# Kernel tuning notes

Measured on AMD Instinct MI355X. Metric: run time of the kernel, lower is better.

## Reference

```python
import jax, jax.numpy as jnp
import numpy as np

N_NODES = 50000
N_EDGES = 1600000
N_GRAPHS = 512
IN_DIM = 128
HID = 128          # nb_hidden
HALF = HID // 2    # per-branch GAT out dim
NEG_SLOPE = 0.2


def _glorot(key, shape):
    fan_in, fan_out = shape[0], shape[-1]
    lim = (6.0 / (fan_in + fan_out)) ** 0.5
    return jax.random.uniform(key, shape, jnp.float32, -lim, lim)


def setup_inputs() -> dict:
    key = jax.random.key(0)
    ks = jax.random.split(key, 32)
    inp = {
        "x": jax.random.normal(ks[0], (N_NODES, IN_DIM), jnp.float32),
        "edge_index": jax.random.randint(ks[1], (2, N_EDGES), 0, N_NODES, jnp.int64),
        "dense_edge_idx": jax.random.randint(ks[2], (2, N_EDGES), 0, N_NODES, jnp.int64),
        "batch": jnp.sort(jax.random.randint(ks[3], (N_NODES,), 0, N_GRAPHS, jnp.int64)),
    }
    # Shared GAT layers (layersB aliases layersA in the source!), nb_layer = 3
    in_dims = [IN_DIM, HID, HID]
    for i, d_in in enumerate(in_dims):
        inp[f"W{i}"] = _glorot(ks[4 + 4 * i], (d_in, HALF))
        inp[f"a_src{i}"] = _glorot(ks[5 + 4 * i], (1, HALF))[0]
        inp[f"a_dst{i}"] = _glorot(ks[6 + 4 * i], (1, HALF))[0]
        inp[f"b{i}"] = jnp.zeros((HALF,), jnp.float32)
    inp["Wf"] = _glorot(ks[20], (HID, 1))
    inp["bf"] = jnp.zeros((1,), jnp.float32)
    return inp


def _gat_conv(x, src, dst, W, a_src, a_dst, b):
    """PyG GATConv, heads=1, concat=True, add_self_loops=True."""
    n = x.shape[0]
    h = x @ W                                   # [N, HALF]
    loops = jnp.arange(n, dtype=src.dtype)
    s = jnp.concatenate([src, loops])           # [E+N]
    d = jnp.concatenate([dst, loops])
    e = (h @ a_src)[s] + (h @ a_dst)[d]         # per-edge raw score
    e = jnp.where(e >= 0, e, NEG_SLOPE * e)     # LeakyReLU(0.2)
    # segment softmax over destination nodes
    m = jax.ops.segment_max(e, d, num_segments=n)
    e = jnp.exp(e - m[d])
    z = jax.ops.segment_sum(e, d, num_segments=n)
    alpha = e / (z[d] + 1e-16)                  # [E+N]
    out = jax.ops.segment_sum(h[s] * alpha[:, None], d, num_segments=n)
    return out + b


def reference(x, edge_index, dense_edge_idx, batch,
              W0, a_src0, a_dst0, b0,
              W1, a_src1, a_dst1, b1,
              W2, a_src2, a_dst2, b2,
              Wf, bf):
    layers = [(W0, a_src0, a_dst0, b0), (W1, a_src1, a_dst1, b1), (W2, a_src2, a_dst2, b2)]
    for (W, a_s, a_d, b) in layers:
        x_A = _gat_conv(x, edge_index[0], edge_index[1], W, a_s, a_d, b)
        x_B = _gat_conv(x, dense_edge_idx[0], dense_edge_idx[1], W, a_s, a_d, b)
        x = jax.nn.relu(jnp.concatenate([x_A, x_B], axis=1))   # [N, HID]
    pooled = jax.ops.segment_sum(x, batch, num_segments=N_GRAPHS)  # [G, HID]
    y = (pooled @ Wf + bf).squeeze(-1)                             # [G]
    return y
```

## Files before the change

kernel.cpp:

```cpp
#include <hip/hip_runtime.h>
#include <hip/hip_bf16.h>
#include <hip/hip_fp16.h>

#define NEG_INF -3.4e38f
#define BCAP 9216

typedef _Float16 f16x8 __attribute__((ext_vector_type(8)));
typedef float f32x4 __attribute__((ext_vector_type(4)));

static __device__ __forceinline__ float leaky(float t) { return t >= 0.f ? t : 0.2f * t; }
static __device__ __forceinline__ float4 h4tof4(uint2 u) {
    float2 f01 = __half22float2(*(__half2*)&u.x);
    float2 f23 = __half22float2(*(__half2*)&u.y);
    return make_float4(f01.x, f01.y, f23.x, f23.y);
}

__global__ __launch_bounds__(256) void bucket_k(const int* __restrict__ eiA, const int* __restrict__ eiB,
                                                int E, int nbkt, int* __restrict__ bktCnt,
                                                int* __restrict__ pairs,
                                                const float* __restrict__ W0, const float* __restrict__ W1,
                                                const float* __restrict__ W2, _Float16* __restrict__ Wt) {
    int t = threadIdx.x;
    if (blockIdx.x < 96) {
        int i = blockIdx.x * 256 + t;
        int l = i >> 13;
        int idx = i & 8191;
        int c = idx >> 7;
        int k = idx & 127;
        const float* W = (l == 0) ? W0 : (l == 1) ? W1 : W2;
        Wt[i] = (_Float16)W[k * 64 + c];
    }

    int KB = gridDim.x >> 1;
    int b = blockIdx.x;
    int sel = (b >= KB);
    int bb = sel ? b - KB : b;
    const int* src = sel ? eiB : eiA;
    const int* dst = src + E;
    int* bc = bktCnt + (sel ? nbkt : 0);
    int* pr = pairs + (size_t)(sel ? nbkt : 0) * BCAP;

    __shared__ int hist[256];
    hist[t] = 0;
    __syncthreads();

    int e0 = (int)(((long long)bb * E) / KB);
    int e1 = (int)(((long long)(bb + 1) * E) / KB);
    for (int i = e0 + t; i < e1; i += 256) atomicAdd(&hist[dst[i] >> 8], 1);
    __syncthreads();

    int h = hist[t];
    int base = h ? atomicAdd(&bc[t], h) : 0;
    __syncthreads();
    hist[t] = base;
    __syncthreads();

    for (int i = e0 + t; i < e1; i += 256) {
        int d = dst[i];
        int s = src[i];
        int bk = d >> 8;
        int pos = atomicAdd(&hist[bk], 1);
        if (pos < BCAP) pr[(size_t)bk * BCAP + pos] = s | ((d & 255) << 16);
    }
}

__global__ __launch_bounds__(256) void bscan_k(const int* __restrict__ bktCnt, const int* __restrict__ pairs,
                                               int N, int nbkt, int2* __restrict__ rpl2,
                                               int* __restrict__ bsum) {
    __shared__ int h[256];
    int b = blockIdx.x;
    int sel = (b >= nbkt);
    int bk = sel ? b - nbkt : b;
    const int* bc = bktCnt + (sel ? nbkt : 0);
    const int* pr = pairs + ((size_t)(sel ? nbkt : 0) + bk) * BCAP;
    int t = threadIdx.x;
    h[t] = 0;
    __syncthreads();
    int cb = min(bc[bk], BCAP);
    for (int i = t; i < cb; i += 256) atomicAdd(&h[pr[i] >> 16], 1);
    __syncthreads();
    int v = h[t];
#pragma unroll
    for (int off = 1; off < 256; off <<= 1) {
        int add = (t >= off) ? h[t - off] : 0;
        __syncthreads();
        h[t] += add;
        __syncthreads();
    }
    int node = (bk << 8) + t;
    if (node < N) rpl2[(sel ? N : 0) + node] = make_int2(h[t] - v, v);
    if (t == 255) bsum[b] = h[255];
}

__global__ __launch_bounds__(512) void scan2_k(int* __restrict__ bsum, int nb,
                                               float* __restrict__ y, const float* __restrict__ bf, int G) {
    __shared__ int s[512];
    int t = threadIdx.x;
    for (int g = t; g < G; g += 512) y[g] = bf[0];
    int seg = t >> 8;
    int j = t & 255;
    int v = (j < nb) ? bsum[seg * nb + j] : 0;
    s[t] = v;
    __syncthreads();
#pragma unroll
    for (int off = 1; off < 256; off <<= 1) {
        int add = (j >= off) ? s[t - off] : 0;
        __syncthreads();
        s[t] += add;
        __syncthreads();
    }
    if (j < nb) bsum[seg * nb + j] = s[t] - v;
}

__global__ __launch_bounds__(256) void bfill2_k(const int* __restrict__ bktCnt, const int* __restrict__ pairs,
                                                int N, int nbkt, const int2* __restrict__ rpl2,
                                                const int* __restrict__ bsum, int4* __restrict__ meta,
                                                int* __restrict__ colA, int* __restrict__ colB) {
    __shared__ int curs[256];
    int b = blockIdx.x;
    int sel = (b >= nbkt);
    int bk = sel ? b - nbkt : b;
    const int* bc = bktCnt + (sel ? nbkt : 0);
    const int* pr = pairs + ((size_t)(sel ? nbkt : 0) + bk) * BCAP;
    int* col = sel ? colB : colA;
    int t = threadIdx.x;
    int base = bsum[b];
    int node = (bk << 8) + t;
    if (node < N) {
        int2 lv = rpl2[(sel ? N : 0) + node];
        int r0 = lv.x + base;
        *(int2*)&meta[(sel ? N : 0) + node] = make_int2(r0, lv.y);
        curs[t] = r0;
    }
    __syncthreads();
    int cb = min(bc[bk], BCAP);
    for (int i = t; i < cb; i += 256) {
        int pk = pr[i];
        int p = atomicAdd(&curs[pk >> 16], 1);
        col[p] = pk & 0xFFFF;
    }
}

template <int IN16>
__global__ __launch_bounds__(256) void gemm_k(const void* __restrict__ Xv, const _Float16* __restrict__ Wt,
                                              const float* __restrict__ asrc, const float* __restrict__ adst,
                                              _Float16* __restrict__ H16, int4* __restrict__ metaA,
                                              int4* __restrict__ metaB, int N) {
    int tid = threadIdx.x;
    int w = tid >> 6;
    int lane = tid & 63;
    int l15 = lane & 15;
    int hi = lane >> 4;
    int rbase = blockIdx.x * 128 + w * 32;

    f32x4 acc[2][4] = {};
#pragma unroll
    for (int kc = 0; kc < 4; ++kc) {
        f16x8 a[2];
#pragma unroll
        for (int mt = 0; mt < 2; ++mt) {
            int r = min(rbase + mt * 16 + l15, N - 1);
            if (IN16) {
                const _Float16* X = (const _Float16*)Xv;
                a[mt] = *(const f16x8*)(X + (size_t)r * 128 + kc * 32 + hi * 8);
            } else {
                const float* px = (const float*)Xv + (size_t)r * 128 + kc * 32 + hi * 8;
                float4 x0 = *(const float4*)px;
                float4 x1 = *(const float4*)(px + 4);
                f16x8 t;
                t[0] = (_Float16)x0.x; t[1] = (_Float16)x0.y; t[2] = (_Float16)x0.z; t[3] = (_Float16)x0.w;
                t[4] = (_Float16)x1.x; t[5] = (_Float16)x1.y; t[6] = (_Float16)x1.z; t[7] = (_Float16)x1.w;
                a[mt] = t;
            }
        }
#pragma unroll
        for (int nt = 0; nt < 4; ++nt) {
            f16x8 bfrag = *(const f16x8*)(Wt + (size_t)(nt * 16 + l15) * 128 + kc * 32 + hi * 8);
            acc[0][nt] = __builtin_amdgcn_mfma_f32_16x16x32_f16(a[0], bfrag, acc[0][nt], 0, 0, 0);
            acc[1][nt] = __builtin_amdgcn_mfma_f32_16x16x32_f16(a[1], bfrag, acc[1][nt], 0, 0, 0);
        }
    }

    float av[4], dv[4];
#pragma unroll
    for (int nt = 0; nt < 4; ++nt) {
        av[nt] = asrc[nt * 16 + l15];
        dv[nt] = adst[nt * 16 + l15];
    }
#pragma unroll
    for (int mt = 0; mt < 2; ++mt) {
#pragma unroll
        for (int r = 0; r < 4; ++r) {
            int row = rbase + mt * 16 + hi * 4 + r;
            float s1 = 0.f, s2 = 0.f;
#pragma unroll
            for (int nt = 0; nt < 4; ++nt) {
                float v = acc[mt][nt][r];
                s1 += v * av[nt];
                s2 += v * dv[nt];
            }
#pragma unroll
            for (int off = 1; off < 16; off <<= 1) {
                s1 += __shfl_xor(s1, off, 64);
                s2 += __shfl_xor(s2, off, 64);
            }
            if (row < N) {
                if (l15 == 0) {
                    float2 sd = make_float2(s1, s2);
                    *(float2*)((char*)&metaA[row] + 8) = sd;
                    *(float2*)((char*)&metaB[row] + 8) = sd;
                }
#pragma unroll
                for (int nt = 0; nt < 4; ++nt)
                    H16[(size_t)row * 64 + nt * 16 + l15] = (_Float16)acc[mt][nt][r];
            }
        }
    }
}

template <int WRITEY>
__global__ __launch_bounds__(256) void agg_k(const _Float16* __restrict__ h16,
                                             const float* __restrict__ asrc,
                                             const int4* __restrict__ metaA, const int* __restrict__ colA,
                                             const int4* __restrict__ metaB, const int* __restrict__ colB,
                                             const float* __restrict__ bias, __half* __restrict__ xout, int N,
                                             const float* __restrict__ Wf,
                                             float* __restrict__ ydotA, float* __restrict__ ydotB) {
    int WBh = gridDim.x >> 1;
    int b = blockIdx.x;
    int sel = (b >= WBh);
    int w = threadIdx.x >> 6;
    int lane = threadIdx.x & 63;
    int wid = (sel ? b - WBh : b) * 4 + w;
    if (wid >= N) return;
    const int4* meta = sel ? metaB : metaA;
    const int* col = sel ? colB : colA;
    int coff = sel ? 64 : 0;

    int q = lane >> 4;
    int l16 = lane & 15;
    int4 mv = meta[wid];
    int r0 = mv.x;
    int deg = mv.y;
    float esv = __int_as_float(mv.z);
    float edv = __int_as_float(mv.w);
    float m = leaky(esv + edv);
    float4 a4 = *(const float4*)(asrc + l16 * 4);

    uint2 hs = *(const uint2*)(h16 + (size_t)wid * 64 + l16 * 4);
    float4 fs = h4tof4(hs);
    float ps = (q == 0) ? 1.f : 0.f;
    float4 acc = make_float4(ps * fs.x, ps * fs.y, ps * fs.z, ps * fs.w);
    float z = ps;

    if (deg > 0) {
        int dm1 = deg - 1;
        int c1 = col[r0 + min(q, dm1)];
        int c2 = col[r0 + min(4 + q, dm1)];
        uint2 h1 = *(const uint2*)(h16 + (size_t)c1 * 64 + l16 * 4);
        uint2 h2 = *(const uint2*)(h16 + (size_t)c2 * 64 + l16 * 4);
        int n1 = col[r0 + min(8 + q, dm1)];
        int n2 = col[r0 + min(12 + q, dm1)];
        for (int j = 0; j < deg; j += 8) {
            uint2 hn1 = *(const uint2*)(h16 + (size_t)n1 * 64 + l16 * 4);
            uint2 hn2 = *(const uint2*)(h16 + (size_t)n2 * 64 + l16 * 4);
            int m1 = col[r0 + min(j + 16 + q, dm1)];
            int m2 = col[r0 + min(j + 20 + q, dm1)];

            float4 f1 = h4tof4(h1);
            float4 f2 = h4tof4(h2);
            float d1 = f1.x * a4.x + f1.y * a4.y + f1.z * a4.z + f1.w * a4.w;
            float d2 = f2.x * a4.x + f2.y * a4.y + f2.z * a4.z + f2.w * a4.w;
#pragma unroll
            for (int off = 1; off < 16; off <<= 1) {
                d1 += __shfl_xor(d1, off, 64);
                d2 += __shfl_xor(d2, off, 64);
            }
            float p1 = (j + q < deg) ? __expf(leaky(d1 + edv) - m) : 0.f;
            float p2 = (j + 4 + q < deg) ? __expf(leaky(d2 + edv) - m) : 0.f;
            z += p1 + p2;
            acc.x = fmaf(p1, f1.x, acc.x);
            acc.y = fmaf(p1, f1.y, acc.y);
            acc.z = fmaf(p1, f1.z, acc.z);
            acc.w = fmaf(p1, f1.w, acc.w);
            acc.x = fmaf(p2, f2.x, acc.x);
            acc.y = fmaf(p2, f2.y, acc.y);
            acc.z = fmaf(p2, f2.z, acc.z);
            acc.w = fmaf(p2, f2.w, acc.w);

            h1 = hn1; h2 = hn2;
            n1 = m1; n2 = m2;
        }
    }

    z += __shfl_xor(z, 16, 64);
    z += __shfl_xor(z, 32, 64);
    acc.x += __shfl_xor(acc.x, 16, 64);
    acc.y += __shfl_xor(acc.y, 16, 64);
    acc.z += __shfl_xor(acc.z, 16, 64);
    acc.w += __shfl_xor(acc.w, 16, 64);
    acc.x += __shfl_xor(acc.x, 32, 64);
    acc.y += __shfl_xor(acc.y, 32, 64);
    acc.z += __shfl_xor(acc.z, 32, 64);
    acc.w += __shfl_xor(acc.w, 32, 64);

    if (q == 0) {
        float inv = 1.f / (z + 1e-16f);
        float4 b4 = *(const float4*)(bias + l16 * 4);
        float4 o;
        o.x = fmaxf(acc.x * inv + b4.x, 0.f);
        o.y = fmaxf(acc.y * inv + b4.y, 0.f);
        o.z = fmaxf(acc.z * inv + b4.z, 0.f);
        o.w = fmaxf(acc.w * inv + b4.w, 0.f);
        if (!WRITEY) {
            __half2 o01 = __floats2half2_rn(o.x, o.y);
            __half2 o23 = __floats2half2_rn(o.z, o.w);
            uint2 st;
            st.x = *(unsigned*)&o01;
            st.y = *(unsigned*)&o23;
            *(uint2*)(xout + (size_t)wid * 128 + coff + l16 * 4) = st;
        } else {
            float4 w4 = *(const float4*)(Wf + coff + l16 * 4);
            float hd = o.x * w4.x + o.y * w4.y + o.z * w4.z + o.w * w4.w;
            hd += __shfl_xor(hd, 1, 64);
            hd += __shfl_xor(hd, 2, 64);
            hd += __shfl_xor(hd, 4, 64);
            hd += __shfl_xor(hd, 8, 64);
            if (l16 == 0) (sel ? ydotB : ydotA)[wid] = hd;
        }
    }
}

__global__ __launch_bounds__(256) void pool3_k(const float* __restrict__ ydotA, const float* __restrict__ ydotB,
                                               const int* __restrict__ batch, float* __restrict__ y,
                                               int N, int G) {
    __shared__ float gacc[512];
    int t = threadIdx.x;
    if (G <= 512) {
        for (int g = t; g < 512; g += 256) gacc[g] = 0.f;
        __syncthreads();
        int n0 = blockIdx.x * 2048 + t * 8;
        int curg = -1;
        float accv = 0.f;
        for (int i = 0; i < 8; ++i) {
            int n = n0 + i;
            if (n < N) {
                float v = ydotA[n] + ydotB[n];
                int g = batch[n];
                if (g == curg) accv += v;
                else {
                    if (curg >= 0) atomicAdd(&gacc[curg], accv);
                    curg = g;
                    accv = v;
                }
            }
        }
        if (curg >= 0) atomicAdd(&gacc[curg], accv);
        __syncthreads();
        for (int g = t; g < G; g += 256) {
            float v = gacc[g];
            if (v != 0.f) atomicAdd(&y[g], v);
        }
    } else {
        int n0 = blockIdx.x * 2048 + t * 8;
        for (int i = 0; i < 8; ++i) {
            int n = n0 + i;
            if (n < N) atomicAdd(&y[batch[n]], ydotA[n] + ydotB[n]);
        }
    }
}

static inline size_t align256(size_t x) { return (x + 255) & ~(size_t)255; }

extern "C" void kernel_launch(void* const* d_in, const int* in_sizes, int n_in,
                              void* d_out, int out_size, void* d_ws, size_t ws_size,
                              hipStream_t stream) {
    const float* x0    = (const float*)d_in[0];
    const int*   eiA   = (const int*)d_in[1];
    const int*   eiB   = (const int*)d_in[2];
    const int*   batch = (const int*)d_in[3];
    const float* W[3]   = {(const float*)d_in[4],  (const float*)d_in[8],  (const float*)d_in[12]};
    const float* as_[3] = {(const float*)d_in[5],  (const float*)d_in[9],  (const float*)d_in[13]};
    const float* ad_[3] = {(const float*)d_in[6],  (const float*)d_in[10], (const float*)d_in[14]};
    const float* bb[3]  = {(const float*)d_in[7],  (const float*)d_in[11], (const float*)d_in[15]};
    const float* Wf = (const float*)d_in[16];
    const float* bf = (const float*)d_in[17];

    const int N = in_sizes[0] / 128;
    const int E = in_sizes[1] / 2;
    const int G = out_size;
    float* y = (float*)d_out;

    const int nbkt = (N + 255) >> 8;
    const int nb = nbkt;

    char* p = (char*)d_ws;
    int2* rpl2  = (int2*)p; p += align256((size_t)2 * N * 8);
    int4* meta  = (int4*)p; p += align256((size_t)2 * N * 16);
    int* bsum   = (int*)p;  p += align256((size_t)2 * nb * 4);
    int* bktCnt = (int*)p;  p += align256((size_t)2 * nbkt * 4);
    int* colA   = (int*)p;  p += align256((size_t)E * 4);
    int* colB   = (int*)p;  p += align256((size_t)E * 4);
    _Float16* h16 = (_Float16*)p; p += align256((size_t)N * 64 * 2);
    float* ydotA = (float*)p; p += align256((size_t)N * 4);
    float* ydotB = (float*)p; p += align256((size_t)N * 4);
    _Float16* Wt = (_Float16*)p; p += align256((size_t)3 * 8192 * 2);
    __half* xb0 = (__half*)p; p += align256((size_t)N * 128 * 2);
    __half* xb1 = (__half*)p; p += align256((size_t)N * 128 * 2);
    int* pairs = (int*)xb0;
    (void)ws_size; (void)n_in;

    const int KB = 256;
    const int WB = (N + 3) / 4;
    const int PB3 = (N + 2047) / 2048;

    hipMemsetAsync(bktCnt, 0, (size_t)2 * nbkt * 4, stream);
    bucket_k<<<2 * KB, 256, 0, stream>>>(eiA, eiB, E, nbkt, bktCnt, pairs, W[0], W[1], W[2], Wt);
    bscan_k<<<2 * nbkt, 256, 0, stream>>>(bktCnt, pairs, N, nbkt, rpl2, bsum);
    scan2_k<<<1, 512, 0, stream>>>(bsum, nb, y, bf, G);
    bfill2_k<<<2 * nbkt, 256, 0, stream>>>(bktCnt, pairs, N, nbkt, rpl2, bsum, meta, colA, colB);

    const int GB = (N + 127) / 128;
    int4* metaA = meta;
    int4* metaB = meta + N;
    gemm_k<0><<<GB, 256, 0, stream>>>(x0, Wt, as_[0], ad_[0], h16, metaA, metaB, N);
    agg_k<0><<<2 * WB, 256, 0, stream>>>(h16, as_[0], metaA, colA, metaB, colB, bb[0], xb0, N,
                                         Wf, ydotA, ydotB);
    gemm_k<1><<<GB, 256, 0, stream>>>(xb0, Wt + 8192, as_[1], ad_[1], h16, metaA, metaB, N);
    agg_k<0><<<2 * WB, 256, 0, stream>>>(h16, as_[1], metaA, colA, metaB, colB, bb[1], xb1, N,
                                         Wf, ydotA, ydotB);
    gemm_k<1><<<GB, 256, 0, stream>>>(xb1, Wt + 16384, as_[2], ad_[2], h16, metaA, metaB, N);
    agg_k<1><<<2 * WB, 256, 0, stream>>>(h16, as_[2], metaA, colA, metaB, colB, bb[2],
                                         (__half*)nullptr, N, Wf, ydotA, ydotB);

    pool3_k<<<PB3, 256, 0, stream>>>(ydotA, ydotB, batch, y, N, G);
}
```

Measured before the change: 335.3 us.

## Use precomputed per-node source scores and merge both graph branches per warp

The aggregation kernel no longer recomputes each neighbor's attention score from its gathered features with a dot product and shuffle reduction. It instead reads a per-node source-score array written by the GEMM. Each warp now handles both edge sets for one node, with grid size halved. Per-edge softmax weights and scaled offsets are staged in shared memory and then consumed in an unrolled gather of four neighbors per quarter-wave. This removes per-edge shuffles and redundant FLOPs and merges the two ydot outputs into one, at the cost of shared-memory staging and a slower fallback path for nodes with degree above 64.

```diff
diff --git a/kernel.cpp b/kernel.cpp
--- a/kernel.cpp
+++ b/kernel.cpp
@@ -114,7 +114,7 @@
 
 __global__ __launch_bounds__(256) void bfill2_k(const int* __restrict__ bktCnt, const int* __restrict__ pairs,
                                                 int N, int nbkt, const int2* __restrict__ rpl2,
-                                                const int* __restrict__ bsum, int4* __restrict__ meta,
+                                                const int* __restrict__ bsum, int2* __restrict__ rp2,
                                                 int* __restrict__ colA, int* __restrict__ colB) {
     __shared__ int curs[256];
     int b = blockIdx.x;
@@ -129,7 +129,7 @@
     if (node < N) {
         int2 lv = rpl2[(sel ? N : 0) + node];
         int r0 = lv.x + base;
-        *(int2*)&meta[(sel ? N : 0) + node] = make_int2(r0, lv.y);
+        rp2[(sel ? N : 0) + node] = make_int2(r0, lv.y);
         curs[t] = r0;
     }
     __syncthreads();
@@ -144,8 +144,8 @@
 template <int IN16>
 __global__ __launch_bounds__(256) void gemm_k(const void* __restrict__ Xv, const _Float16* __restrict__ Wt,
                                               const float* __restrict__ asrc, const float* __restrict__ adst,
-                                              _Float16* __restrict__ H16, int4* __restrict__ metaA,
-                                              int4* __restrict__ metaB, int N) {
+                                              _Float16* __restrict__ H16, float* __restrict__ es,
+                                              float* __restrict__ ed, int N) {
     int tid = threadIdx.x;
     int w = tid >> 6;
     int lane = tid & 63;
@@ -205,11 +205,7 @@
                 s2 += __shfl_xor(s2, off, 64);
             }
             if (row < N) {
-                if (l15 == 0) {
-                    float2 sd = make_float2(s1, s2);
-                    *(float2*)((char*)&metaA[row] + 8) = sd;
-                    *(float2*)((char*)&metaB[row] + 8) = sd;
-                }
+                if (l15 == 0) { es[row] = s1; ed[row] = s2; }
 #pragma unroll
                 for (int nt = 0; nt < 4; ++nt)
                     H16[(size_t)row * 64 + nt * 16 + l15] = (_Float16)acc[mt][nt][r];
@@ -220,118 +216,142 @@
 
 template <int WRITEY>
 __global__ __launch_bounds__(256) void agg_k(const _Float16* __restrict__ h16,
-                                             const float* __restrict__ asrc,
-                                             const int4* __restrict__ metaA, const int* __restrict__ colA,
-                                             const int4* __restrict__ metaB, const int* __restrict__ colB,
+                                             const float* __restrict__ es, const float* __restrict__ ed,
+                                             const int2* __restrict__ rp2A, const int* __restrict__ colA,
+                                             const int2* __restrict__ rp2B, const int* __restrict__ colB,
                                              const float* __restrict__ bias, __half* __restrict__ xout, int N,
-                                             const float* __restrict__ Wf,
-                                             float* __restrict__ ydotA, float* __restrict__ ydotB) {
-    int WBh = gridDim.x >> 1;
-    int b = blockIdx.x;
-    int sel = (b >= WBh);
+                                             const float* __restrict__ Wf, float* __restrict__ ydot) {
+    __shared__ int2 sp[4][2][64];
     int w = threadIdx.x >> 6;
     int lane = threadIdx.x & 63;
-    int wid = (sel ? b - WBh : b) * 4 + w;
+    int wid = blockIdx.x * 4 + w;
     if (wid >= N) return;
-    const int4* meta = sel ? metaB : metaA;
-    const int* col = sel ? colB : colA;
-    int coff = sel ? 64 : 0;
-
     int q = lane >> 4;
     int l16 = lane & 15;
-    int4 mv = meta[wid];
-    int r0 = mv.x;
-    int deg = mv.y;
-    float esv = __int_as_float(mv.z);
-    float edv = __int_as_float(mv.w);
-    float m = leaky(esv + edv);
-    float4 a4 = *(const float4*)(asrc + l16 * 4);
-
-    uint2 hs = *(const uint2*)(h16 + (size_t)wid * 64 + l16 * 4);
+    int2 ra = rp2A[wid];
+    int2 rb = rp2B[wid];
+    float edv = ed[wid];
+    float m = leaky(es[wid] + edv);
+    const char* hb = (const char*)h16;
+    int loff = l16 * 8;
+
+    uint2 hs = *(const uint2*)(hb + (((size_t)wid) << 7) + loff);
     float4 fs = h4tof4(hs);
-    float ps = (q == 0) ? 1.f : 0.f;
-    float4 acc = make_float4(ps * fs.x, ps * fs.y, ps * fs.z, ps * fs.w);
-    float z = ps;
-
-    if (deg > 0) {
-        int dm1 = deg - 1;
-        int c1 = col[r0 + min(q, dm1)];
-        int c2 = col[r0 + min(4 + q, dm1)];
-        uint2 h1 = *(const uint2*)(h16 + (size_t)c1 * 64 + l16 * 4);
-        uint2 h2 = *(const uint2*)(h16 + (size_t)c2 * 64 + l16 * 4);
-        int n1 = col[r0 + min(8 + q, dm1)];
-        int n2 = col[r0 + min(12 + q, dm1)];
-        for (int j = 0; j < deg; j += 8) {
-            uint2 hn1 = *(const uint2*)(h16 + (size_t)n1 * 64 + l16 * 4);
-            uint2 hn2 = *(const uint2*)(h16 + (size_t)n2 * 64 + l16 * 4);
-            int m1 = col[r0 + min(j + 16 + q, dm1)];
-            int m2 = col[r0 + min(j + 20 + q, dm1)];
-
-            float4 f1 = h4tof4(h1);
-            float4 f2 = h4tof4(h2);
-            float d1 = f1.x * a4.x + f1.y * a4.y + f1.z * a4.z + f1.w * a4.w;
-            float d2 = f2.x * a4.x + f2.y * a4.y + f2.z * a4.z + f2.w * a4.w;
-#pragma unroll
-            for (int off = 1; off < 16; off <<= 1) {
-                d1 += __shfl_xor(d1, off, 64);
-                d2 += __shfl_xor(d2, off, 64);
-            }
-            float p1 = (j + q < deg) ? __expf(leaky(d1 + edv) - m) : 0.f;
-            float p2 = (j + 4 + q < deg) ? __expf(leaky(d2 + edv) - m) : 0.f;
-            z += p1 + p2;
-            acc.x = fmaf(p1, f1.x, acc.x);
-            acc.y = fmaf(p1, f1.y, acc.y);
-            acc.z = fmaf(p1, f1.z, acc.z);
-            acc.w = fmaf(p1, f1.w, acc.w);
-            acc.x = fmaf(p2, f2.x, acc.x);
-            acc.y = fmaf(p2, f2.y, acc.y);
-            acc.z = fmaf(p2, f2.z, acc.z);
-            acc.w = fmaf(p2, f2.w, acc.w);
-
-            h1 = hn1; h2 = hn2;
-            n1 = m1; n2 = m2;
-        }
-    }
-
-    z += __shfl_xor(z, 16, 64);
-    z += __shfl_xor(z, 32, 64);
-    acc.x += __shfl_xor(acc.x, 16, 64);
-    acc.y += __shfl_xor(acc.y, 16, 64);
-    acc.z += __shfl_xor(acc.z, 16, 64);
-    acc.w += __shfl_xor(acc.w, 16, 64);
-    acc.x += __shfl_xor(acc.x, 32, 64);
-    acc.y += __shfl_xor(acc.y, 32, 64);
-    acc.z += __shfl_xor(acc.z, 32, 64);
-    acc.w += __shfl_xor(acc.w, 32, 64);
+    float s0 = (q == 0) ? 1.f : 0.f;
+    float4 accA = make_float4(s0 * fs.x, s0 * fs.y, s0 * fs.z, s0 * fs.w);
+    float4 accB = accA;
+    float zA = s0, zB = s0;
+
+#define GATHER16(SPW, ACC, ZV, RR)                                           \
+    for (int j = 0; j < (RR); j += 16) {                                     \
+        int2 e1 = (SPW)[j + q];                                              \
+        int2 e2 = (SPW)[j + 4 + q];                                          \
+        int2 e3 = (SPW)[j + 8 + q];                                          \
+        int2 e4 = (SPW)[j + 12 + q];                                         \
+        uint2 u1 = *(const uint2*)(hb + (unsigned)(e1.x + loff));            \
+        uint2 u2 = *(const uint2*)(hb + (unsigned)(e2.x + loff));            \
+        uint2 u3 = *(const uint2*)(hb + (unsigned)(e3.x + loff));            \
+        uint2 u4 = *(const uint2*)(hb + (unsigned)(e4.x + loff));            \
+        float p1 = __int_as_float(e1.y), p2 = __int_as_float(e2.y);          \
+        float p3 = __int_as_float(e3.y), p4 = __int_as_float(e4.y);          \
+        float4 f1 = h4tof4(u1), f2 = h4tof4(u2), f3 = h4tof4(u3), f4 = h4tof4(u4); \
+        ZV += (p1 + p2) + (p3 + p4);                                         \
+        ACC.x = fmaf(p1, f1.x, ACC.x); ACC.y = fmaf(p1, f1.y, ACC.y);        \
+        ACC.z = fmaf(p1, f1.z, ACC.z); ACC.w = fmaf(p1, f1.w, ACC.w);        \
+        ACC.x = fmaf(p2, f2.x, ACC.x); ACC.y = fmaf(p2, f2.y, ACC.y);        \
+        ACC.z = fmaf(p2, f2.z, ACC.z); ACC.w = fmaf(p2, f2.w, ACC.w);        \
+        ACC.x = fmaf(p3, f3.x, ACC.x); ACC.y = fmaf(p3, f3.y, ACC.y);        \
+        ACC.z = fmaf(p3, f3.z, ACC.z); ACC.w = fmaf(p3, f3.w, ACC.w);        \
+        ACC.x = fmaf(p4, f4.x, ACC.x); ACC.y = fmaf(p4, f4.y, ACC.y);        \
+        ACC.z = fmaf(p4, f4.z, ACC.z); ACC.w = fmaf(p4, f4.w, ACC.w);        \
+    }
+
+    if (ra.y <= 64 && rb.y <= 64) {
+        int svA = (lane < ra.y) ? colA[ra.x + lane] : wid;
+        int svB = (lane < rb.y) ? colB[rb.x + lane] : wid;
+        float eA = es[svA];
+        float eB = es[svB];
+        float pA = (lane < ra.y) ? __expf(leaky(eA + edv) - m) : 0.f;
+        float pB = (lane < rb.y) ? __expf(leaky(eB + edv) - m) : 0.f;
+        sp[w][0][lane] = make_int2(svA << 7, __float_as_int(pA));
+        sp[w][1][lane] = make_int2(svB << 7, __float_as_int(pB));
+        int rrA = ((ra.y + 15) >> 4) << 4;
+        int rrB = ((rb.y + 15) >> 4) << 4;
+        GATHER16(sp[w][0], accA, zA, rrA)
+        GATHER16(sp[w][1], accB, zB, rrB)
+    } else {
+        for (int base = 0; base < ra.y; base += 64) {
+            int vi = base + lane;
+            int sv = (vi < ra.y) ? colA[ra.x + vi] : wid;
+            float e = es[sv];
+            float p = (vi < ra.y) ? __expf(leaky(e + edv) - m) : 0.f;
+            sp[w][0][lane] = make_int2(sv << 7, __float_as_int(p));
+            int cw = min(64, ra.y - base);
+            int rr = ((cw + 15) >> 4) << 4;
+            GATHER16(sp[w][0], accA, zA, rr)
+        }
+        for (int base = 0; base < rb.y; base += 64) {
+            int vi = base + lane;
+            int sv = (vi < rb.y) ? colB[rb.x + vi] : wid;
+            float e = es[sv];
+            float p = (vi < rb.y) ? __expf(leaky(e + edv) - m) : 0.f;
+            sp[w][1][lane] = make_int2(sv << 7, __float_as_int(p));
+            int cw = min(64, rb.y - base);
+            int rr = ((cw + 15) >> 4) << 4;
+            GATHER16(sp[w][1], accB, zB, rr)
+        }
+    }
+#undef GATHER16
+
+    zA += __shfl_xor(zA, 16, 64); zA += __shfl_xor(zA, 32, 64);
+    zB += __shfl_xor(zB, 16, 64); zB += __shfl_xor(zB, 32, 64);
+    accA.x += __shfl_xor(accA.x, 16, 64); accA.x += __shfl_xor(accA.x, 32, 64);
+    accA.y += __shfl_xor(accA.y, 16, 64); accA.y += __shfl_xor(accA.y, 32, 64);
+    accA.z += __shfl_xor(accA.z, 16, 64); accA.z += __shfl_xor(accA.z, 32, 64);
+    accA.w += __shfl_xor(accA.w, 16, 64); accA.w += __shfl_xor(accA.w, 32, 64);
+    accB.x += __shfl_xor(accB.x, 16, 64); accB.x += __shfl_xor(accB.x, 32, 64);
+    accB.y += __shfl_xor(accB.y, 16, 64); accB.y += __shfl_xor(accB.y, 32, 64);
+    accB.z += __shfl_xor(accB.z, 16, 64); accB.z += __shfl_xor(accB.z, 32, 64);
+    accB.w += __shfl_xor(accB.w, 16, 64); accB.w += __shfl_xor(accB.w, 32, 64);
 
     if (q == 0) {
-        float inv = 1.f / (z + 1e-16f);
+        float invA = 1.f / (zA + 1e-16f);
+        float invB = 1.f / (zB + 1e-16f);
         float4 b4 = *(const float4*)(bias + l16 * 4);
-        float4 o;
-        o.x = fmaxf(acc.x * inv + b4.x, 0.f);
-        o.y = fmaxf(acc.y * inv + b4.y, 0.f);
-        o.z = fmaxf(acc.z * inv + b4.z, 0.f);
-        o.w = fmaxf(acc.w * inv + b4.w, 0.f);
+        float4 oA, oB;
+        oA.x = fmaxf(accA.x * invA + b4.x, 0.f);
+        oA.y = fmaxf(accA.y * invA + b4.y, 0.f);
+        oA.z = fmaxf(accA.z * invA + b4.z, 0.f);
+        oA.w = fmaxf(accA.w * invA + b4.w, 0.f);
+        oB.x = fmaxf(accB.x * invB + b4.x, 0.f);
+        oB.y = fmaxf(accB.y * invB + b4.y, 0.f);
+        oB.z = fmaxf(accB.z * invB + b4.z, 0.f);
+        oB.w = fmaxf(accB.w * invB + b4.w, 0.f);
         if (!WRITEY) {
-            __half2 o01 = __floats2half2_rn(o.x, o.y);
-            __half2 o23 = __floats2half2_rn(o.z, o.w);
-            uint2 st;
-            st.x = *(unsigned*)&o01;
-            st.y = *(unsigned*)&o23;
-            *(uint2*)(xout + (size_t)wid * 128 + coff + l16 * 4) = st;
+            __half2 a01 = __floats2half2_rn(oA.x, oA.y);
+            __half2 a23 = __floats2half2_rn(oA.z, oA.w);
+            __half2 b01 = __floats2half2_rn(oB.x, oB.y);
+            __half2 b23 = __floats2half2_rn(oB.z, oB.w);
+            uint2 stA, stB;
+            stA.x = *(unsigned*)&a01; stA.y = *(unsigned*)&a23;
+            stB.x = *(unsigned*)&b01; stB.y = *(unsigned*)&b23;
+            *(uint2*)(xout + (size_t)wid * 128 + l16 * 4) = stA;
+            *(uint2*)(xout + (size_t)wid * 128 + 64 + l16 * 4) = stB;
         } else {
-            float4 w4 = *(const float4*)(Wf + coff + l16 * 4);
-            float hd = o.x * w4.x + o.y * w4.y + o.z * w4.z + o.w * w4.w;
+            float4 wA = *(const float4*)(Wf + l16 * 4);
+            float4 wB = *(const float4*)(Wf + 64 + l16 * 4);
+            float hd = oA.x * wA.x + oA.y * wA.y + oA.z * wA.z + oA.w * wA.w
+                     + oB.x * wB.x + oB.y * wB.y + oB.z * wB.z + oB.w * wB.w;
             hd += __shfl_xor(hd, 1, 64);
             hd += __shfl_xor(hd, 2, 64);
             hd += __shfl_xor(hd, 4, 64);
             hd += __shfl_xor(hd, 8, 64);
-            if (l16 == 0) (sel ? ydotB : ydotA)[wid] = hd;
-        }
-    }
-}
-
-__global__ __launch_bounds__(256) void pool3_k(const float* __restrict__ ydotA, const float* __restrict__ ydotB,
+            if (l16 == 0) ydot[wid] = hd;
+        }
+    }
+}
+
+__global__ __launch_bounds__(256) void pool3_k(const float* __restrict__ ydot,
                                                const int* __restrict__ batch, float* __restrict__ y,
                                                int N, int G) {
     __shared__ float gacc[512];
@@ -345,7 +365,7 @@
         for (int i = 0; i < 8; ++i) {
             int n = n0 + i;
             if (n < N) {
-                float v = ydotA[n] + ydotB[n];
+                float v = ydot[n];
                 int g = batch[n];
                 if (g == curg) accv += v;
                 else {
@@ -365,7 +385,7 @@
         int n0 = blockIdx.x * 2048 + t * 8;
         for (int i = 0; i < 8; ++i) {
             int n = n0 + i;
-            if (n < N) atomicAdd(&y[batch[n]], ydotA[n] + ydotB[n]);
+            if (n < N) atomicAdd(&y[batch[n]], ydot[n]);
         }
     }
 }
@@ -396,14 +416,15 @@
 
     char* p = (char*)d_ws;
     int2* rpl2  = (int2*)p; p += align256((size_t)2 * N * 8);
-    int4* meta  = (int4*)p; p += align256((size_t)2 * N * 16);
+    int2* rp2   = (int2*)p; p += align256((size_t)2 * N * 8);
     int* bsum   = (int*)p;  p += align256((size_t)2 * nb * 4);
     int* bktCnt = (int*)p;  p += align256((size_t)2 * nbkt * 4);
     int* colA   = (int*)p;  p += align256((size_t)E * 4);
     int* colB   = (int*)p;  p += align256((size_t)E * 4);
     _Float16* h16 = (_Float16*)p; p += align256((size_t)N * 64 * 2);
-    float* ydotA = (float*)p; p += align256((size_t)N * 4);
-    float* ydotB = (float*)p; p += align256((size_t)N * 4);
+    float* es   = (float*)p; p += align256((size_t)N * 4);
+    float* ed   = (float*)p; p += align256((size_t)N * 4);
+    float* ydot = (float*)p; p += align256((size_t)N * 4);
     _Float16* Wt = (_Float16*)p; p += align256((size_t)3 * 8192 * 2);
     __half* xb0 = (__half*)p; p += align256((size_t)N * 128 * 2);
     __half* xb1 = (__half*)p; p += align256((size_t)N * 128 * 2);
@@ -418,20 +439,17 @@
     bucket_k<<<2 * KB, 256, 0, stream>>>(eiA, eiB, E, nbkt, bktCnt, pairs, W[0], W[1], W[2], Wt);
     bscan_k<<<2 * nbkt, 256, 0, stream>>>(bktCnt, pairs, N, nbkt, rpl2, bsum);
     scan2_k<<<1, 512, 0, stream>>>(bsum, nb, y, bf, G);
-    bfill2_k<<<2 * nbkt, 256, 0, stream>>>(bktCnt, pairs, N, nbkt, rpl2, bsum, meta, colA, colB);
+    bfill2_k<<<2 * nbkt, 256, 0, stream>>>(bktCnt, pairs, N, nbkt, rpl2, bsum, rp2, colA, colB);
 
     const int GB = (N + 127) / 128;
-    int4* metaA = meta;
-    int4* metaB = meta + N;
-    gemm_k<0><<<GB, 256, 0, stream>>>(x0, Wt, as_[0], ad_[0], h16, metaA, metaB, N);
-    agg_k<0><<<2 * WB, 256, 0, stream>>>(h16, as_[0], metaA, colA, metaB, colB, bb[0], xb0, N,
-                                         Wf, ydotA, ydotB);
-    gemm_k<1><<<GB, 256, 0, stream>>>(xb0, Wt + 8192, as_[1], ad_[1], h16, metaA, metaB, N);
-    agg_k<0><<<2 * WB, 256, 0, stream>>>(h16, as_[1], metaA, colA, metaB, colB, bb[1], xb1, N,
-                                         Wf, ydotA, ydotB);
-    gemm_k<1><<<GB, 256, 0, stream>>>(xb1, Wt + 16384, as_[2], ad_[2], h16, metaA, metaB, N);
-    agg_k<1><<<2 * WB, 256, 0, stream>>>(h16, as_[2], metaA, colA, metaB, colB, bb[2],
-                                         (__half*)nullptr, N, Wf, ydotA, ydotB);
-
-    pool3_k<<<PB3, 256, 0, stream>>>(ydotA, ydotB, batch, y, N, G);
-}
+    const int2* rp2A = rp2;
+    const int2* rp2B = rp2 + N;
+    gemm_k<0><<<GB, 256, 0, stream>>>(x0, Wt, as_[0], ad_[0], h16, es, ed, N);
+    agg_k<0><<<WB, 256, 0, stream>>>(h16, es, ed, rp2A, colA, rp2B, colB, bb[0], xb0, N, Wf, ydot);
+    gemm_k<1><<<GB, 256, 0, stream>>>(xb0, Wt + 8192, as_[1], ad_[1], h16, es, ed, N);
+    agg_k<0><<<WB, 256, 0, stream>>>(h16, es, ed, rp2A, colA, rp2B, colB, bb[1], xb1, N, Wf, ydot);
+    gemm_k<1><<<GB, 256, 0, stream>>>(xb1, Wt + 16384, as_[2], ad_[2], h16, es, ed, N);
+    agg_k<1><<<WB, 256, 0, stream>>>(h16, es, ed, rp2A, colA, rp2B, colB, bb[2], (__half*)nullptr, N, Wf, ydot);
+
+    pool3_k<<<PB3, 256, 0, stream>>>(ydot, batch, y, N, G);
+}
```

Result: faster. 274.7 us (-18.1%).
